# Performance work log

Measured on AMD Instinct MI355X. Metric: run time of the kernel, lower is better.

Reference implementation:

```python
import jax, jax.numpy as jnp
import numpy as np
from jax import lax


def setup_inputs() -> dict:
    key = jax.random.key(0)
    ks = jax.random.split(key, 6)
    B, S, V, E, H = 256, 512, 50000, 100, 512
    sentence = jax.random.randint(ks[0], (B, S), 0, V, dtype=jnp.int64)
    emb = jax.random.normal(ks[1], (V, E), dtype=jnp.float32)
    s = 1.0 / np.sqrt(H)
    W_ih = jax.random.normal(ks[2], (4 * H, E), dtype=jnp.float32) * s
    W_hh = jax.random.normal(ks[3], (4 * H, H), dtype=jnp.float32) * s
    b_ih = jax.random.normal(ks[4], (4 * H,), dtype=jnp.float32) * s
    b_hh = jax.random.normal(ks[5], (4 * H,), dtype=jnp.float32) * s
    return {"sentence": sentence, "emb": emb, "W_ih": W_ih, "W_hh": W_hh,
            "b_ih": b_ih, "b_hh": b_hh}


def reference(sentence, emb, W_ih, W_hh, b_ih, b_hh):
    # sentence: [B, S] int -> embed -> transpose to [S, B, E] (seq-major LSTM)
    x = jnp.take(emb, sentence, axis=0)            # [B, S, E]
    x = jnp.transpose(x, (1, 0, 2))                # [S, B, E]
    B = x.shape[1]
    H = W_hh.shape[1]
    # Precompute input contribution for all timesteps (big batched GEMM).
    # PyTorch gate layout along 4H axis: i, f, g, o.
    xg = jnp.einsum('sbe,ge->sbg', x, W_ih) + b_ih + b_hh  # [S, B, 4H]

    def step(carry, xt):
        h, c = carry
        gates = xt + h @ W_hh.T                    # [B, 4H]
        i, f, g, o = jnp.split(gates, 4, axis=-1)
        i = jax.nn.sigmoid(i)
        f = jax.nn.sigmoid(f)
        g = jnp.tanh(g)
        o = jax.nn.sigmoid(o)
        c = f * c + i * g
        h = o * jnp.tanh(c)
        return (h, c), None

    h0 = jnp.zeros((B, H), dtype=x.dtype)
    c0 = jnp.zeros((B, H), dtype=x.dtype)
    (hT, _), _ = lax.scan(step, (h0, c0), xg)
    # lstm_out[-1] is the hidden state at the final timestep.
    return hT
```

## Files before the change

### kernel.cpp

```cpp
#include <hip/hip_runtime.h>
#include <stdint.h>

#define B_  256
#define S_  512
#define E_  100
#define H_  512
#define G_  2048
#define KH_ 512

typedef _Float16 half8 __attribute__((ext_vector_type(8)));
typedef float    f32x4 __attribute__((ext_vector_type(4)));
union V16 { f32x4 f; half8 h; unsigned long long q[2]; };

#define OFF_WC   0u
#define OFF_HBT  2621440u
#define OFF_XB3  3670016u
#define OFF_XTL  28835840u
#define OFF_BIAS 29884416u
#define WS_NEED  29892608u

#define LDS_W   131072
#define LDS_A   16384
#define LDS_G   8448
#define LDS_TOT (LDS_W + LDS_A + LDS_G)

__global__ void prep_wc4(const float* __restrict__ Wih, const float* __restrict__ Whh,
                         const float* __restrict__ bih, const float* __restrict__ bhh,
                         _Float16* __restrict__ Wc, float* __restrict__ bias) {
    int idx = blockIdx.x * 256 + threadIdx.x;
    int e  = idx & 7;
    int L  = (idx >> 3) & 63;
    int q  = idx >> 9;
    int s  = q % 20;
    int qq = q / 20;
    int n  = qq & 1;
    int w  = (qq >> 1) & 3;
    int c  = qq >> 3;
    int g  = (w << 9) + (c << 5) + (n << 4) + (L & 15);
    int kl = ((L >> 4) << 3) + e;
    float v = 0.f;
    if (s < 16) {
        v = Whh[g * KH_ + (s << 5) + kl];
    } else {
        int xk = (s < 19) ? ((s - 16) << 5) + kl : 96 + kl;
        if (xk < E_) v = Wih[g * E_ + xk];
    }
    Wc[idx] = (_Float16)v;
    if (idx < G_) bias[idx] = bih[idx] + bhh[idx];
}

__global__ void prep_x3(const int* __restrict__ sent, const float* __restrict__ emb,
                        _Float16* __restrict__ xb3) {
    size_t idx = (size_t)blockIdx.x * 256 + threadIdx.x;
    int e  = (int)(idx & 7);
    int L  = (int)((idx >> 3) & 63);
    int q  = (int)(idx >> 9);
    int j  = q % 3;
    int qq = q / 3;
    int rg = qq & 15;
    int t  = qq >> 4;
    int b  = (rg << 4) + (L & 15);
    int k  = (j << 5) + ((L >> 4) << 3) + e;
    int tok = sent[b * S_ + t];
    xb3[idx] = (_Float16)emb[(size_t)tok * E_ + k];
}

__global__ void prep_xtail(const int* __restrict__ sent, const float* __restrict__ emb,
                           _Float16* __restrict__ xtl) {
    int idx = blockIdx.x * 256 + threadIdx.x;
    int e = idx & 3;
    int b = (idx >> 2) & 255;
    int t = idx >> 10;
    int tok = sent[b * S_ + t];
    xtl[idx] = (_Float16)emb[(size_t)tok * E_ + 96 + e];
}

__global__ __launch_bounds__(256, 1) void lstm_persist(
    const _Float16* __restrict__ Wc, unsigned long long* __restrict__ hbt,
    const _Float16* __restrict__ xb3, const _Float16* __restrict__ xtl,
    const float* __restrict__ bias, float* __restrict__ out)
{
    extern __shared__ __align__(16) char smem[];
    char* wl = smem;
    char* al = smem + LDS_W;
    float (*gbuf)[16][33] = reinterpret_cast<float(*)[16][33]>(smem + LDS_W + LDS_A);

    const int tid = threadIdx.x;
    const int L   = tid & 63;
    const int w   = tid >> 6;
    const int bx  = blockIdx.x;
    const int xcd = bx & 7;
    const int kk_ = bx >> 3;
    const int r   = (xcd << 1) | (kk_ >> 4);
    const int c   = kk_ & 15;
    const int brow0 = r << 4;
    const int hcol0 = c << 5;

    const _Float16* wp0 = Wc + (size_t)((((c << 2) + w) << 1)) * (20 * 512) + (L << 3);
    const _Float16* wp1 = wp0 + 20 * 512;
#pragma unroll
    for (int n = 0; n < 2; ++n)
#pragma unroll
        for (int kt = 0; kt < 16; ++kt) {
            f32x4 v = *reinterpret_cast<const f32x4*>((n ? wp1 : wp0) + (kt << 9));
            *reinterpret_cast<f32x4*>(wl + ((((w << 1) + n) * 16 + kt) << 10) + (L << 4)) = v;
        }
    V16 wx[2][4];
#pragma unroll
    for (int n = 0; n < 2; ++n)
#pragma unroll
        for (int j = 0; j < 4; ++j)
            wx[n][j].f = *reinterpret_cast<const f32x4*>((n ? wp1 : wp0) + ((16 + j) << 9));

    const int bl = tid >> 4;
    const int j0 = (tid << 1) & 31;
    const float bi0 = bias[hcol0 + j0],         bi1 = bias[hcol0 + j0 + 1];
    const float bf0 = bias[512  + hcol0 + j0],  bf1 = bias[512  + hcol0 + j0 + 1];
    const float bg0 = bias[1024 + hcol0 + j0],  bg1 = bias[1024 + hcol0 + j0 + 1];
    const float bo0 = bias[1536 + hcol0 + j0],  bo1 = bias[1536 + hcol0 + j0 + 1];
    float cc0 = 0.f, cc1 = 0.f;

    const int arow = L & 15;
    const int agrp = L >> 4;
    const int ard  = arow << 10;
    const int asw  = (arow & 7) << 4;

    V16 xf[3], xt;
    {
        const _Float16* xp = xb3 + ((size_t)r * 3) * 512 + (L << 3);
#pragma unroll
        for (int j = 0; j < 3; ++j) xf[j].f = *reinterpret_cast<const f32x4*>(xp + j * 512);
        unsigned long long tv = *reinterpret_cast<const unsigned long long*>(
            xtl + (size_t)(brow0 + arow) * 4);
        xt.q[0] = (agrp == 0) ? tv : 0ull;
        xt.q[1] = 0ull;
    }

    for (int t = 0; t < S_; ++t) {
        f32x4 a00 = {0,0,0,0}, a01 = {0,0,0,0}, a10 = {0,0,0,0}, a11 = {0,0,0,0};
#pragma unroll
        for (int j = 0; j < 4; ++j) {
            half8 a = (j < 3) ? xf[j].h : xt.h;
            if (j & 1) {
                a01 = __builtin_amdgcn_mfma_f32_16x16x32_f16(a, wx[0][j].h, a01, 0, 0, 0);
                a11 = __builtin_amdgcn_mfma_f32_16x16x32_f16(a, wx[1][j].h, a11, 0, 0, 0);
            } else {
                a00 = __builtin_amdgcn_mfma_f32_16x16x32_f16(a, wx[0][j].h, a00, 0, 0, 0);
                a10 = __builtin_amdgcn_mfma_f32_16x16x32_f16(a, wx[1][j].h, a10, 0, 0, 0);
            }
        }

        if (t > 0) {
            const unsigned long long* hq = hbt + ((size_t)(t & 1) << 16) + ((size_t)brow0 << 8);
            const unsigned tag = (unsigned)t;
            unsigned long long vv[16];
            int rounds = 0;
            bool again = true;
            while (again) {
#pragma unroll
                for (int j = 0; j < 16; ++j)
                    vv[j] = __hip_atomic_load(hq + (j << 8) + tid,
                                              __ATOMIC_RELAXED, __HIP_MEMORY_SCOPE_AGENT);
                again = false;
#pragma unroll
                for (int j = 0; j < 16; ++j) again |= ((unsigned)vv[j] != tag);
                if (++rounds > 4000000) break;
            }
            __builtin_amdgcn_sched_barrier(0);
#pragma unroll
            for (int j = 0; j < 16; ++j) {
                unsigned pack = (unsigned)(vv[j] >> 32);
                *reinterpret_cast<unsigned*>(
                    al + (j << 10) + ((((tid >> 2) ^ (j & 7))) << 4) + ((tid & 3) << 2)) = pack;
            }
        }
        __syncthreads();

        if (t > 0) {
#pragma unroll
            for (int kt = 0; kt < 16; ++kt) {
                V16 av, b0, b1;
                av.f = *reinterpret_cast<const f32x4*>(
                    al + ard + ((((kt << 2) + agrp) << 4) ^ asw));
                b0.f = *reinterpret_cast<const f32x4*>(wl + (((w << 5) + kt) << 10) + (L << 4));
                b1.f = *reinterpret_cast<const f32x4*>(wl + (((w << 5) + 16 + kt) << 10) + (L << 4));
                if (kt & 1) {
                    a01 = __builtin_amdgcn_mfma_f32_16x16x32_f16(av.h, b0.h, a01, 0, 0, 0);
                    a11 = __builtin_amdgcn_mfma_f32_16x16x32_f16(av.h, b1.h, a11, 0, 0, 0);
                } else {
                    a00 = __builtin_amdgcn_mfma_f32_16x16x32_f16(av.h, b0.h, a00, 0, 0, 0);
                    a10 = __builtin_amdgcn_mfma_f32_16x16x32_f16(av.h, b1.h, a10, 0, 0, 0);
                }
            }
        }
        f32x4 g0 = a00 + a01;
        f32x4 g1 = a10 + a11;
        {
            const int grb = agrp << 2;
            const int gc  = L & 15;
#pragma unroll
            for (int rr = 0; rr < 4; ++rr) {
                gbuf[w][grb + rr][gc]      = g0[rr];
                gbuf[w][grb + rr][16 + gc] = g1[rr];
            }
        }

        V16 xn[3], xnt;
        {
            const int tn = (t + 1) & (S_ - 1);
            const _Float16* xp = xb3 + (((size_t)tn * 16 + r) * 3) * 512 + (L << 3);
#pragma unroll
            for (int j = 0; j < 3; ++j) xn[j].f = *reinterpret_cast<const f32x4*>(xp + j * 512);
            unsigned long long tv = *reinterpret_cast<const unsigned long long*>(
                xtl + ((size_t)tn * 256 + brow0 + arow) * 4);
            xnt.q[0] = (agrp == 0) ? tv : 0ull;
            xnt.q[1] = 0ull;
        }
        __syncthreads();

        float i0 = gbuf[0][bl][j0]     + bi0, i1 = gbuf[0][bl][j0 + 1] + bi1;
        float f0 = gbuf[1][bl][j0]     + bf0, f1 = gbuf[1][bl][j0 + 1] + bf1;
        float gg0= gbuf[2][bl][j0]     + bg0, gg1= gbuf[2][bl][j0 + 1] + bg1;
        float o0 = gbuf[3][bl][j0]     + bo0, o1 = gbuf[3][bl][j0 + 1] + bo1;
        float si0 = 1.f / (1.f + __expf(-i0));
        float sf0 = 1.f / (1.f + __expf(-f0));
        float so0 = 1.f / (1.f + __expf(-o0));
        float tg0 = tanhf(gg0);
        float si1 = 1.f / (1.f + __expf(-i1));
        float sf1 = 1.f / (1.f + __expf(-f1));
        float so1 = 1.f / (1.f + __expf(-o1));
        float tg1 = tanhf(gg1);
        cc0 = sf0 * cc0 + si0 * tg0;
        cc1 = sf1 * cc1 + si1 * tg1;
        float h0 = so0 * tanhf(cc0);
        float h1 = so1 * tanhf(cc1);

        if (t == S_ - 1) {
            float* op = out + (size_t)(brow0 + bl) * H_ + hcol0 + j0;
            op[0] = h0; op[1] = h1;
        } else {
            _Float16 hh0 = (_Float16)h0, hh1 = (_Float16)h1;
            unsigned pack = ((unsigned)*(unsigned short*)&hh1 << 16)
                          |  (unsigned)*(unsigned short*)&hh0;
            unsigned long long word = ((unsigned long long)pack << 32)
                                    |  (unsigned long long)(unsigned)(t + 1);
            __hip_atomic_store(hbt + ((size_t)((t + 1) & 1) << 16)
                                   + ((size_t)(brow0 + bl) << 8) + (c << 4) + (tid & 15),
                               word, __ATOMIC_RELAXED, __HIP_MEMORY_SCOPE_AGENT);
        }

#pragma unroll
        for (int j = 0; j < 3; ++j) xf[j] = xn[j];
        xt = xnt;
    }
}

extern "C" void kernel_launch(void* const* d_in, const int* in_sizes, int n_in,
                              void* d_out, int out_size, void* d_ws, size_t ws_size,
                              hipStream_t stream) {
    (void)in_sizes; (void)n_in; (void)out_size;
    if (ws_size < WS_NEED) return;

    const int*   sent = (const int*)d_in[0];
    const float* emb  = (const float*)d_in[1];
    const float* Wih  = (const float*)d_in[2];
    const float* Whh  = (const float*)d_in[3];
    const float* bih  = (const float*)d_in[4];
    const float* bhh  = (const float*)d_in[5];

    char* ws = (char*)d_ws;
    _Float16*           Wc   = (_Float16*)(ws + OFF_WC);
    unsigned long long* hbt  = (unsigned long long*)(ws + OFF_HBT);
    _Float16*           xb3  = (_Float16*)(ws + OFF_XB3);
    _Float16*           xtl  = (_Float16*)(ws + OFF_XTL);
    float*              bias = (float*)(ws + OFF_BIAS);

    (void)hipFuncSetAttribute(reinterpret_cast<const void*>(lstm_persist),
                              hipFuncAttributeMaxDynamicSharedMemorySize, LDS_TOT);

    (void)hipMemsetAsync(hbt, 0, 2 * 256 * 256 * sizeof(unsigned long long), stream);

    prep_wc4<<<(16 * 4 * 2 * 20 * 64 * 8) / 256, 256, 0, stream>>>(Wih, Whh, bih, bhh, Wc, bias);
    prep_x3<<<(S_ * 16 * 3 * 512) / 256, 256, 0, stream>>>(sent, emb, xb3);
    prep_xtail<<<(S_ * B_ * 4) / 256, 256, 0, stream>>>(sent, emb, xtl);
    lstm_persist<<<256, 256, LDS_TOT, stream>>>(Wc, hbt, xb3, xtl, bias, (float*)d_out);
}
```

Baseline: 1.304 ms.

## Keep half of recurrent weights in registers and prefetch hidden-state polls early

Half of each wave's W_hh tiles (the first 8 k-steps) now stay in VGPRs and only the other half go to LDS, which halves LDS weight traffic per step and the LDS allocation. The hidden-state poll is restructured: the first load of the next step's h values is issued right after this step's store, a check runs before any reload, and s_sleep backs off between retries. The goal is to hide some of the cross-workgroup synchronisation latency and reduce polling pressure on memory, at the cost of higher register pressure and possible extra wake-up latency from the sleep.

```diff
diff --git a/kernel.cpp b/kernel.cpp
--- a/kernel.cpp
+++ b/kernel.cpp
@@ -19,7 +19,7 @@
 #define OFF_BIAS 29884416u
 #define WS_NEED  29892608u
 
-#define LDS_W   131072
+#define LDS_W   65536
 #define LDS_A   16384
 #define LDS_G   8448
 #define LDS_TOT (LDS_W + LDS_A + LDS_G)
@@ -75,7 +75,8 @@
     xtl[idx] = (_Float16)emb[(size_t)tok * E_ + 96 + e];
 }
 
-__global__ __launch_bounds__(256, 1) void lstm_persist(
+__global__ __launch_bounds__(256) __attribute__((amdgpu_waves_per_eu(1, 1)))
+void lstm_persist(
     const _Float16* __restrict__ Wc, unsigned long long* __restrict__ hbt,
     const _Float16* __restrict__ xb3, const _Float16* __restrict__ xtl,
     const float* __restrict__ bias, float* __restrict__ out)
@@ -98,13 +99,24 @@
 
     const _Float16* wp0 = Wc + (size_t)((((c << 2) + w) << 1)) * (20 * 512) + (L << 3);
     const _Float16* wp1 = wp0 + 20 * 512;
+    V16 wr[2][8];
 #pragma unroll
     for (int n = 0; n < 2; ++n)
 #pragma unroll
         for (int kt = 0; kt < 16; ++kt) {
             f32x4 v = *reinterpret_cast<const f32x4*>((n ? wp1 : wp0) + (kt << 9));
-            *reinterpret_cast<f32x4*>(wl + ((((w << 1) + n) * 16 + kt) << 10) + (L << 4)) = v;
-        }
+            if (kt < 8) {
+                wr[n][kt].f = v;
+            } else {
+                *reinterpret_cast<f32x4*>(
+                    wl + ((((w << 1) + n) << 3 | (kt - 8)) << 10) + (L << 4)) = v;
+            }
+        }
+#pragma unroll
+    for (int n = 0; n < 2; ++n)
+#pragma unroll
+        for (int kt = 0; kt < 8; ++kt)
+            asm volatile("" : "+v"(wr[n][kt].f));
     V16 wx[2][4];
 #pragma unroll
     for (int n = 0; n < 2; ++n)
@@ -135,6 +147,8 @@
         xt.q[0] = (agrp == 0) ? tv : 0ull;
         xt.q[1] = 0ull;
     }
+
+    unsigned long long vv[16];
 
     for (int t = 0; t < S_; ++t) {
         f32x4 a00 = {0,0,0,0}, a01 = {0,0,0,0}, a10 = {0,0,0,0}, a11 = {0,0,0,0};
@@ -153,18 +167,18 @@
         if (t > 0) {
             const unsigned long long* hq = hbt + ((size_t)(t & 1) << 16) + ((size_t)brow0 << 8);
             const unsigned tag = (unsigned)t;
-            unsigned long long vv[16];
             int rounds = 0;
-            bool again = true;
-            while (again) {
+            for (;;) {
+                bool again = false;
+#pragma unroll
+                for (int j = 0; j < 16; ++j) again |= ((unsigned)vv[j] != tag);
+                if (!again) break;
+                if (++rounds > 2000000) break;
+                __builtin_amdgcn_s_sleep(1);
 #pragma unroll
                 for (int j = 0; j < 16; ++j)
                     vv[j] = __hip_atomic_load(hq + (j << 8) + tid,
                                               __ATOMIC_RELAXED, __HIP_MEMORY_SCOPE_AGENT);
-                again = false;
-#pragma unroll
-                for (int j = 0; j < 16; ++j) again |= ((unsigned)vv[j] != tag);
-                if (++rounds > 4000000) break;
             }
             __builtin_amdgcn_sched_barrier(0);
 #pragma unroll
@@ -182,8 +196,15 @@
                 V16 av, b0, b1;
                 av.f = *reinterpret_cast<const f32x4*>(
                     al + ard + ((((kt << 2) + agrp) << 4) ^ asw));
-                b0.f = *reinterpret_cast<const f32x4*>(wl + (((w << 5) + kt) << 10) + (L << 4));
-                b1.f = *reinterpret_cast<const f32x4*>(wl + (((w << 5) + 16 + kt) << 10) + (L << 4));
+                if (kt < 8) {
+                    b0 = wr[0][kt];
+                    b1 = wr[1][kt];
+                } else {
+                    b0.f = *reinterpret_cast<const f32x4*>(
+                        wl + ((((w << 1) | 0) << 3 | (kt - 8)) << 10) + (L << 4));
+                    b1.f = *reinterpret_cast<const f32x4*>(
+                        wl + ((((w << 1) | 1) << 3 | (kt - 8)) << 10) + (L << 4));
+                }
                 if (kt & 1) {
                     a01 = __builtin_amdgcn_mfma_f32_16x16x32_f16(av.h, b0.h, a01, 0, 0, 0);
                     a11 = __builtin_amdgcn_mfma_f32_16x16x32_f16(av.h, b1.h, a11, 0, 0, 0);
@@ -247,6 +268,12 @@
             __hip_atomic_store(hbt + ((size_t)((t + 1) & 1) << 16)
                                    + ((size_t)(brow0 + bl) << 8) + (c << 4) + (tid & 15),
                                word, __ATOMIC_RELAXED, __HIP_MEMORY_SCOPE_AGENT);
+            const unsigned long long* hq2 = hbt + ((size_t)((t + 1) & 1) << 16)
+                                                + ((size_t)brow0 << 8);
+#pragma unroll
+            for (int j = 0; j < 16; ++j)
+                vv[j] = __hip_atomic_load(hq2 + (j << 8) + tid,
+                                          __ATOMIC_RELAXED, __HIP_MEMORY_SCOPE_AGENT);
         }
 
 #pragma unroll
```

Result: slower. 2.142 ms (+64.3%).

## Split each block over two row groups and overlap h exchange with compute

Applied to the files above, without the earlier changes.

Each persistent block now owns 16 hidden columns for two 16-row batch groups, where before it owned 32 columns for a single group. The two groups are processed in an interleaved pipeline: while one group's gate MFMAs and activations run, the other group's hidden state is prefetched with inline-asm cache-bypassing loads and checked against a tag, with a retry loop. The hidden-state exchange format shrinks to 32-bit words holding an fp16 value and a 16-bit tag, and the LDS weight footprint is halved. The intent is to hide cross-block synchronization latency behind compute, at the cost of more barriers per step and inline-asm memory-ordering risk.

```diff
diff --git a/kernel.cpp b/kernel.cpp
--- a/kernel.cpp
+++ b/kernel.cpp
@@ -10,7 +10,10 @@
 
 typedef _Float16 half8 __attribute__((ext_vector_type(8)));
 typedef float    f32x4 __attribute__((ext_vector_type(4)));
+typedef unsigned uint4v __attribute__((ext_vector_type(4)));
 union V16 { f32x4 f; half8 h; unsigned long long q[2]; };
+
+#define MFMA16 __builtin_amdgcn_mfma_f32_16x16x32_f16
 
 #define OFF_WC   0u
 #define OFF_HBT  2621440u
@@ -19,12 +22,72 @@
 #define OFF_BIAS 29884416u
 #define WS_NEED  29892608u
 
-#define LDS_W   131072
+#define LDS_W   65536
 #define LDS_A   16384
-#define LDS_G   8448
+#define LDS_G   4352
 #define LDS_TOT (LDS_W + LDS_A + LDS_G)
 
-__global__ void prep_wc4(const float* __restrict__ Wih, const float* __restrict__ Whh,
+#define GL8(v, b)                                                       \
+  asm volatile(                                                         \
+    "global_load_dwordx4 %0, %8, off sc0 sc1\n\t"                       \
+    "global_load_dwordx4 %1, %9, off sc0 sc1\n\t"                       \
+    "global_load_dwordx4 %2, %10, off sc0 sc1\n\t"                      \
+    "global_load_dwordx4 %3, %11, off sc0 sc1\n\t"                      \
+    "global_load_dwordx4 %4, %12, off sc0 sc1\n\t"                      \
+    "global_load_dwordx4 %5, %13, off sc0 sc1\n\t"                      \
+    "global_load_dwordx4 %6, %14, off sc0 sc1\n\t"                      \
+    "global_load_dwordx4 %7, %15, off sc0 sc1"                          \
+    : "=&v"(v[0]), "=&v"(v[1]), "=&v"(v[2]), "=&v"(v[3]),               \
+      "=&v"(v[4]), "=&v"(v[5]), "=&v"(v[6]), "=&v"(v[7])                \
+    : "v"(b), "v"(b + 4096), "v"(b + 8192), "v"(b + 12288),             \
+      "v"(b + 16384), "v"(b + 20480), "v"(b + 24576), "v"(b + 28672)    \
+    : "memory")
+
+#define GL8W(v, b)                                                      \
+  asm volatile(                                                         \
+    "global_load_dwordx4 %0, %8, off sc0 sc1\n\t"                       \
+    "global_load_dwordx4 %1, %9, off sc0 sc1\n\t"                       \
+    "global_load_dwordx4 %2, %10, off sc0 sc1\n\t"                      \
+    "global_load_dwordx4 %3, %11, off sc0 sc1\n\t"                      \
+    "global_load_dwordx4 %4, %12, off sc0 sc1\n\t"                      \
+    "global_load_dwordx4 %5, %13, off sc0 sc1\n\t"                      \
+    "global_load_dwordx4 %6, %14, off sc0 sc1\n\t"                      \
+    "global_load_dwordx4 %7, %15, off sc0 sc1\n\t"                      \
+    "s_waitcnt vmcnt(0)"                                                \
+    : "=&v"(v[0]), "=&v"(v[1]), "=&v"(v[2]), "=&v"(v[3]),               \
+      "=&v"(v[4]), "=&v"(v[5]), "=&v"(v[6]), "=&v"(v[7])                \
+    : "v"(b), "v"(b + 4096), "v"(b + 8192), "v"(b + 12288),             \
+      "v"(b + 16384), "v"(b + 20480), "v"(b + 24576), "v"(b + 28672)    \
+    : "memory")
+
+#define VWAIT8(v)                                                       \
+  asm volatile("s_waitcnt vmcnt(0)"                                     \
+    : "+v"(v[0]), "+v"(v[1]), "+v"(v[2]), "+v"(v[3]),                   \
+      "+v"(v[4]), "+v"(v[5]), "+v"(v[6]), "+v"(v[7]) :: "memory")
+
+static __device__ __forceinline__ void validate_retry(uint4v* v, const char* base,
+                                                      unsigned tag) {
+    VWAIT8(v);
+    __builtin_amdgcn_sched_barrier(0);
+    unsigned bad = 0;
+#pragma unroll
+    for (int i = 0; i < 8; ++i)
+#pragma unroll
+        for (int k = 0; k < 4; ++k) bad |= (v[i][k] ^ tag) & 0xFFFFu;
+    int r = 0;
+    while (__any(bad != 0)) {
+        if (++r > 2000000) break;
+        GL8W(v, base);
+        bad = 0;
+#pragma unroll
+        for (int i = 0; i < 8; ++i)
+#pragma unroll
+            for (int k = 0; k < 4; ++k) bad |= (v[i][k] ^ tag) & 0xFFFFu;
+    }
+    __builtin_amdgcn_sched_barrier(0);
+}
+
+__global__ void prep_wc5(const float* __restrict__ Wih, const float* __restrict__ Whh,
                          const float* __restrict__ bih, const float* __restrict__ bhh,
                          _Float16* __restrict__ Wc, float* __restrict__ bias) {
     int idx = blockIdx.x * 256 + threadIdx.x;
@@ -32,11 +95,10 @@
     int L  = (idx >> 3) & 63;
     int q  = idx >> 9;
     int s  = q % 20;
-    int qq = q / 20;
-    int n  = qq & 1;
-    int w  = (qq >> 1) & 3;
-    int c  = qq >> 3;
-    int g  = (w << 9) + (c << 5) + (n << 4) + (L & 15);
+    int r1 = q / 20;
+    int w  = r1 & 3;
+    int c  = r1 >> 2;
+    int g  = (w << 9) + (c << 4) + (L & 15);
     int kl = ((L >> 4) << 3) + e;
     float v = 0.f;
     if (s < 16) {
@@ -76,183 +138,217 @@
 }
 
 __global__ __launch_bounds__(256, 1) void lstm_persist(
-    const _Float16* __restrict__ Wc, unsigned long long* __restrict__ hbt,
+    const _Float16* __restrict__ Wc, unsigned* __restrict__ hbt,
     const _Float16* __restrict__ xb3, const _Float16* __restrict__ xtl,
     const float* __restrict__ bias, float* __restrict__ out)
 {
     extern __shared__ __align__(16) char smem[];
     char* wl = smem;
     char* al = smem + LDS_W;
-    float (*gbuf)[16][33] = reinterpret_cast<float(*)[16][33]>(smem + LDS_W + LDS_A);
+    float (*gbuf)[16][17] = reinterpret_cast<float(*)[16][17]>(smem + LDS_W + LDS_A);
 
     const int tid = threadIdx.x;
     const int L   = tid & 63;
     const int w   = tid >> 6;
     const int bx  = blockIdx.x;
-    const int xcd = bx & 7;
-    const int kk_ = bx >> 3;
-    const int r   = (xcd << 1) | (kk_ >> 4);
-    const int c   = kk_ & 15;
-    const int brow0 = r << 4;
-    const int hcol0 = c << 5;
-
-    const _Float16* wp0 = Wc + (size_t)((((c << 2) + w) << 1)) * (20 * 512) + (L << 3);
-    const _Float16* wp1 = wp0 + 20 * 512;
-#pragma unroll
-    for (int n = 0; n < 2; ++n)
-#pragma unroll
-        for (int kt = 0; kt < 16; ++kt) {
-            f32x4 v = *reinterpret_cast<const f32x4*>((n ? wp1 : wp0) + (kt << 9));
-            *reinterpret_cast<f32x4*>(wl + ((((w << 1) + n) * 16 + kt) << 10) + (L << 4)) = v;
-        }
-    V16 wx[2][4];
-#pragma unroll
-    for (int n = 0; n < 2; ++n)
-#pragma unroll
-        for (int j = 0; j < 4; ++j)
-            wx[n][j].f = *reinterpret_cast<const f32x4*>((n ? wp1 : wp0) + ((16 + j) << 9));
-
-    const int bl = tid >> 4;
-    const int j0 = (tid << 1) & 31;
-    const float bi0 = bias[hcol0 + j0],         bi1 = bias[hcol0 + j0 + 1];
-    const float bf0 = bias[512  + hcol0 + j0],  bf1 = bias[512  + hcol0 + j0 + 1];
-    const float bg0 = bias[1024 + hcol0 + j0],  bg1 = bias[1024 + hcol0 + j0 + 1];
-    const float bo0 = bias[1536 + hcol0 + j0],  bo1 = bias[1536 + hcol0 + j0 + 1];
-    float cc0 = 0.f, cc1 = 0.f;
+    const int rp  = bx & 7;
+    const int c16 = bx >> 3;
+    const int rA  = rp, rB = rp + 8;
+    const int hcol0 = c16 << 4;
+
+    const _Float16* wp = Wc + (size_t)((c16 << 2) + w) * (20 * 512) + (L << 3);
+#pragma unroll
+    for (int s = 0; s < 16; ++s)
+        *reinterpret_cast<f32x4*>(wl + (((w << 4) + s) << 10) + (L << 4)) =
+            *reinterpret_cast<const f32x4*>(wp + (s << 9));
+    V16 wx[4];
+#pragma unroll
+    for (int j = 0; j < 4; ++j)
+        wx[j].f = *reinterpret_cast<const f32x4*>(wp + ((16 + j) << 9));
+
+    const int eb = tid >> 4;
+    const int ej = tid & 15;
+    const int hcol = hcol0 + ej;
+    const float bi = bias[hcol], bf = bias[512 + hcol];
+    const float bg = bias[1024 + hcol], bo = bias[1536 + hcol];
+    float csA = 0.f, csB = 0.f;
 
     const int arow = L & 15;
     const int agrp = L >> 4;
     const int ard  = arow << 10;
     const int asw  = (arow & 7) << 4;
 
-    V16 xf[3], xt;
+    V16 xfA[3], xtA, xfB[3], xtB, xnA[3], xntA, xnB[3], xntB;
     {
-        const _Float16* xp = xb3 + ((size_t)r * 3) * 512 + (L << 3);
-#pragma unroll
-        for (int j = 0; j < 3; ++j) xf[j].f = *reinterpret_cast<const f32x4*>(xp + j * 512);
-        unsigned long long tv = *reinterpret_cast<const unsigned long long*>(
-            xtl + (size_t)(brow0 + arow) * 4);
-        xt.q[0] = (agrp == 0) ? tv : 0ull;
-        xt.q[1] = 0ull;
+        const _Float16* xpA = xb3 + ((size_t)rA * 3) * 512 + (L << 3);
+        const _Float16* xpB = xb3 + ((size_t)rB * 3) * 512 + (L << 3);
+#pragma unroll
+        for (int j = 0; j < 3; ++j) {
+            xfA[j].f = *reinterpret_cast<const f32x4*>(xpA + j * 512);
+            xfB[j].f = *reinterpret_cast<const f32x4*>(xpB + j * 512);
+        }
+        unsigned long long tvA = *reinterpret_cast<const unsigned long long*>(
+            xtl + (size_t)(rA * 16 + arow) * 4);
+        unsigned long long tvB = *reinterpret_cast<const unsigned long long*>(
+            xtl + (size_t)(rB * 16 + arow) * 4);
+        xtA.q[0] = (agrp == 0) ? tvA : 0ull;  xtA.q[1] = 0ull;
+        xtB.q[0] = (agrp == 0) ? tvB : 0ull;  xtB.q[1] = 0ull;
     }
 
+    uint4v vA[8] = {}, vB[8] = {};
+
+#define STAGE8(v)                                                            \
+    do {                                                                     \
+        _Pragma("unroll")                                                    \
+        for (int i = 0; i < 8; ++i) {                                        \
+            int b_ = (i << 1) + (tid >> 7);                                  \
+            unsigned lo = (v[i][0] >> 16) | (v[i][1] & 0xFFFF0000u);         \
+            unsigned hi = (v[i][2] >> 16) | (v[i][3] & 0xFFFF0000u);         \
+            unsigned long long val = ((unsigned long long)hi << 32) | lo;    \
+            *reinterpret_cast<unsigned long long*>(                          \
+                al + (b_ << 10) +                                            \
+                (((((tid & 127) >> 1) << 4) ^ ((b_ & 7) << 4))) +            \
+                ((tid & 1) << 3)) = val;                                     \
+        }                                                                    \
+    } while (0)
+
     for (int t = 0; t < S_; ++t) {
-        f32x4 a00 = {0,0,0,0}, a01 = {0,0,0,0}, a10 = {0,0,0,0}, a11 = {0,0,0,0};
-#pragma unroll
-        for (int j = 0; j < 4; ++j) {
-            half8 a = (j < 3) ? xf[j].h : xt.h;
-            if (j & 1) {
-                a01 = __builtin_amdgcn_mfma_f32_16x16x32_f16(a, wx[0][j].h, a01, 0, 0, 0);
-                a11 = __builtin_amdgcn_mfma_f32_16x16x32_f16(a, wx[1][j].h, a11, 0, 0, 0);
+        const char* baseA_t  = (const char*)hbt + ((size_t)(t & 1) << 19)
+                             + ((size_t)rA << 15) + (tid << 4);
+        const char* baseB_t  = (const char*)hbt + ((size_t)(t & 1) << 19)
+                             + ((size_t)rB << 15) + (tid << 4);
+        const unsigned tag = (unsigned)t;
+
+        if (t > 0) { validate_retry(vA, baseA_t, tag); STAGE8(vA); }
+        __syncthreads();
+        if (t > 0) { GL8(vB, baseB_t); __builtin_amdgcn_sched_barrier(0); }
+
+        {
+            f32x4 a0 = {0,0,0,0}, a1 = {0,0,0,0};
+#pragma unroll
+            for (int j = 0; j < 4; ++j) {
+                half8 a = (j < 3) ? xfA[j].h : xtA.h;
+                if (j & 1) a1 = MFMA16(a, wx[j].h, a1, 0, 0, 0);
+                else       a0 = MFMA16(a, wx[j].h, a0, 0, 0, 0);
+            }
+            if (t > 0) {
+#pragma unroll
+                for (int kt = 0; kt < 16; ++kt) {
+                    V16 av, bv;
+                    av.f = *reinterpret_cast<const f32x4*>(
+                        al + ard + ((((kt << 2) + agrp) << 4) ^ asw));
+                    bv.f = *reinterpret_cast<const f32x4*>(
+                        wl + (((w << 4) + kt) << 10) + (L << 4));
+                    if (kt & 1) a1 = MFMA16(av.h, bv.h, a1, 0, 0, 0);
+                    else        a0 = MFMA16(av.h, bv.h, a0, 0, 0, 0);
+                }
+            }
+            f32x4 g = a0 + a1;
+            const int grb = agrp << 2, gc = L & 15;
+#pragma unroll
+            for (int rr = 0; rr < 4; ++rr) gbuf[w][grb + rr][gc] = g[rr];
+        }
+        __syncthreads();
+
+        {
+            float iv = gbuf[0][eb][ej] + bi, fv = gbuf[1][eb][ej] + bf;
+            float gv = gbuf[2][eb][ej] + bg, ov = gbuf[3][eb][ej] + bo;
+            float si = 1.f / (1.f + __expf(-iv));
+            float sf = 1.f / (1.f + __expf(-fv));
+            float so = 1.f / (1.f + __expf(-ov));
+            float tg = tanhf(gv);
+            csA = sf * csA + si * tg;
+            float hv = so * tanhf(csA);
+            if (t == S_ - 1) {
+                out[(size_t)(rA * 16 + eb) * H_ + hcol] = hv;
             } else {
-                a00 = __builtin_amdgcn_mfma_f32_16x16x32_f16(a, wx[0][j].h, a00, 0, 0, 0);
-                a10 = __builtin_amdgcn_mfma_f32_16x16x32_f16(a, wx[1][j].h, a10, 0, 0, 0);
-            }
-        }
-
-        if (t > 0) {
-            const unsigned long long* hq = hbt + ((size_t)(t & 1) << 16) + ((size_t)brow0 << 8);
-            const unsigned tag = (unsigned)t;
-            unsigned long long vv[16];
-            int rounds = 0;
-            bool again = true;
-            while (again) {
-#pragma unroll
-                for (int j = 0; j < 16; ++j)
-                    vv[j] = __hip_atomic_load(hq + (j << 8) + tid,
-                                              __ATOMIC_RELAXED, __HIP_MEMORY_SCOPE_AGENT);
-                again = false;
-#pragma unroll
-                for (int j = 0; j < 16; ++j) again |= ((unsigned)vv[j] != tag);
-                if (++rounds > 4000000) break;
-            }
+                _Float16 hh = (_Float16)hv;
+                unsigned word = ((unsigned)*(unsigned short*)&hh << 16)
+                              | (unsigned)(t + 1);
+                __hip_atomic_store(hbt + ((size_t)((t + 1) & 1) << 17)
+                                       + ((size_t)rA << 13) + (eb << 9) + hcol,
+                                   word, __ATOMIC_RELAXED, __HIP_MEMORY_SCOPE_AGENT);
+            }
+        }
+
+        if (t > 0) { validate_retry(vB, baseB_t, tag); STAGE8(vB); }
+        __syncthreads();
+        if (t < S_ - 1) {
+            const char* baseA_n = (const char*)hbt + ((size_t)((t + 1) & 1) << 19)
+                                + ((size_t)rA << 15) + (tid << 4);
+            GL8(vA, baseA_n);
             __builtin_amdgcn_sched_barrier(0);
-#pragma unroll
-            for (int j = 0; j < 16; ++j) {
-                unsigned pack = (unsigned)(vv[j] >> 32);
-                *reinterpret_cast<unsigned*>(
-                    al + (j << 10) + ((((tid >> 2) ^ (j & 7))) << 4) + ((tid & 3) << 2)) = pack;
-            }
+        }
+        {
+            const int tn = (t + 1) & (S_ - 1);
+            const _Float16* xpA = xb3 + (((size_t)tn * 16 + rA) * 3) * 512 + (L << 3);
+            const _Float16* xpB = xb3 + (((size_t)tn * 16 + rB) * 3) * 512 + (L << 3);
+#pragma unroll
+            for (int j = 0; j < 3; ++j) {
+                xnA[j].f = *reinterpret_cast<const f32x4*>(xpA + j * 512);
+                xnB[j].f = *reinterpret_cast<const f32x4*>(xpB + j * 512);
+            }
+            unsigned long long tvA = *reinterpret_cast<const unsigned long long*>(
+                xtl + ((size_t)tn * 256 + rA * 16 + arow) * 4);
+            unsigned long long tvB = *reinterpret_cast<const unsigned long long*>(
+                xtl + ((size_t)tn * 256 + rB * 16 + arow) * 4);
+            xntA.q[0] = (agrp == 0) ? tvA : 0ull;  xntA.q[1] = 0ull;
+            xntB.q[0] = (agrp == 0) ? tvB : 0ull;  xntB.q[1] = 0ull;
+        }
+
+        {
+            f32x4 a0 = {0,0,0,0}, a1 = {0,0,0,0};
+#pragma unroll
+            for (int j = 0; j < 4; ++j) {
+                half8 a = (j < 3) ? xfB[j].h : xtB.h;
+                if (j & 1) a1 = MFMA16(a, wx[j].h, a1, 0, 0, 0);
+                else       a0 = MFMA16(a, wx[j].h, a0, 0, 0, 0);
+            }
+            if (t > 0) {
+#pragma unroll
+                for (int kt = 0; kt < 16; ++kt) {
+                    V16 av, bv;
+                    av.f = *reinterpret_cast<const f32x4*>(
+                        al + ard + ((((kt << 2) + agrp) << 4) ^ asw));
+                    bv.f = *reinterpret_cast<const f32x4*>(
+                        wl + (((w << 4) + kt) << 10) + (L << 4));
+                    if (kt & 1) a1 = MFMA16(av.h, bv.h, a1, 0, 0, 0);
+                    else        a0 = MFMA16(av.h, bv.h, a0, 0, 0, 0);
+                }
+            }
+            f32x4 g = a0 + a1;
+            const int grb = agrp << 2, gc = L & 15;
+#pragma unroll
+            for (int rr = 0; rr < 4; ++rr) gbuf[w][grb + rr][gc] = g[rr];
         }
         __syncthreads();
 
-        if (t > 0) {
-#pragma unroll
-            for (int kt = 0; kt < 16; ++kt) {
-                V16 av, b0, b1;
-                av.f = *reinterpret_cast<const f32x4*>(
-                    al + ard + ((((kt << 2) + agrp) << 4) ^ asw));
-                b0.f = *reinterpret_cast<const f32x4*>(wl + (((w << 5) + kt) << 10) + (L << 4));
-                b1.f = *reinterpret_cast<const f32x4*>(wl + (((w << 5) + 16 + kt) << 10) + (L << 4));
-                if (kt & 1) {
-                    a01 = __builtin_amdgcn_mfma_f32_16x16x32_f16(av.h, b0.h, a01, 0, 0, 0);
-                    a11 = __builtin_amdgcn_mfma_f32_16x16x32_f16(av.h, b1.h, a11, 0, 0, 0);
-                } else {
-                    a00 = __builtin_amdgcn_mfma_f32_16x16x32_f16(av.h, b0.h, a00, 0, 0, 0);
-                    a10 = __builtin_amdgcn_mfma_f32_16x16x32_f16(av.h, b1.h, a10, 0, 0, 0);
-                }
-            }
-        }
-        f32x4 g0 = a00 + a01;
-        f32x4 g1 = a10 + a11;
-        {
-            const int grb = agrp << 2;
-            const int gc  = L & 15;
-#pragma unroll
-            for (int rr = 0; rr < 4; ++rr) {
-                gbuf[w][grb + rr][gc]      = g0[rr];
-                gbuf[w][grb + rr][16 + gc] = g1[rr];
-            }
-        }
-
-        V16 xn[3], xnt;
-        {
-            const int tn = (t + 1) & (S_ - 1);
-            const _Float16* xp = xb3 + (((size_t)tn * 16 + r) * 3) * 512 + (L << 3);
-#pragma unroll
-            for (int j = 0; j < 3; ++j) xn[j].f = *reinterpret_cast<const f32x4*>(xp + j * 512);
-            unsigned long long tv = *reinterpret_cast<const unsigned long long*>(
-                xtl + ((size_t)tn * 256 + brow0 + arow) * 4);
-            xnt.q[0] = (agrp == 0) ? tv : 0ull;
-            xnt.q[1] = 0ull;
-        }
-        __syncthreads();
-
-        float i0 = gbuf[0][bl][j0]     + bi0, i1 = gbuf[0][bl][j0 + 1] + bi1;
-        float f0 = gbuf[1][bl][j0]     + bf0, f1 = gbuf[1][bl][j0 + 1] + bf1;
-        float gg0= gbuf[2][bl][j0]     + bg0, gg1= gbuf[2][bl][j0 + 1] + bg1;
-        float o0 = gbuf[3][bl][j0]     + bo0, o1 = gbuf[3][bl][j0 + 1] + bo1;
-        float si0 = 1.f / (1.f + __expf(-i0));
-        float sf0 = 1.f / (1.f + __expf(-f0));
-        float so0 = 1.f / (1.f + __expf(-o0));
-        float tg0 = tanhf(gg0);
-        float si1 = 1.f / (1.f + __expf(-i1));
-        float sf1 = 1.f / (1.f + __expf(-f1));
-        float so1 = 1.f / (1.f + __expf(-o1));
-        float tg1 = tanhf(gg1);
-        cc0 = sf0 * cc0 + si0 * tg0;
-        cc1 = sf1 * cc1 + si1 * tg1;
-        float h0 = so0 * tanhf(cc0);
-        float h1 = so1 * tanhf(cc1);
-
-        if (t == S_ - 1) {
-            float* op = out + (size_t)(brow0 + bl) * H_ + hcol0 + j0;
-            op[0] = h0; op[1] = h1;
-        } else {
-            _Float16 hh0 = (_Float16)h0, hh1 = (_Float16)h1;
-            unsigned pack = ((unsigned)*(unsigned short*)&hh1 << 16)
-                          |  (unsigned)*(unsigned short*)&hh0;
-            unsigned long long word = ((unsigned long long)pack << 32)
-                                    |  (unsigned long long)(unsigned)(t + 1);
-            __hip_atomic_store(hbt + ((size_t)((t + 1) & 1) << 16)
-                                   + ((size_t)(brow0 + bl) << 8) + (c << 4) + (tid & 15),
-                               word, __ATOMIC_RELAXED, __HIP_MEMORY_SCOPE_AGENT);
-        }
-
-#pragma unroll
-        for (int j = 0; j < 3; ++j) xf[j] = xn[j];
-        xt = xnt;
+        {
+            float iv = gbuf[0][eb][ej] + bi, fv = gbuf[1][eb][ej] + bf;
+            float gv = gbuf[2][eb][ej] + bg, ov = gbuf[3][eb][ej] + bo;
+            float si = 1.f / (1.f + __expf(-iv));
+            float sf = 1.f / (1.f + __expf(-fv));
+            float so = 1.f / (1.f + __expf(-ov));
+            float tg = tanhf(gv);
+            csB = sf * csB + si * tg;
+            float hv = so * tanhf(csB);
+            if (t == S_ - 1) {
+                out[(size_t)(rB * 16 + eb) * H_ + hcol] = hv;
+            } else {
+                _Float16 hh = (_Float16)hv;
+                unsigned word = ((unsigned)*(unsigned short*)&hh << 16)
+                              | (unsigned)(t + 1);
+                __hip_atomic_store(hbt + ((size_t)((t + 1) & 1) << 17)
+                                       + ((size_t)rB << 13) + (eb << 9) + hcol,
+                                   word, __ATOMIC_RELAXED, __HIP_MEMORY_SCOPE_AGENT);
+            }
+        }
+
+#pragma unroll
+        for (int j = 0; j < 3; ++j) { xfA[j] = xnA[j]; xfB[j] = xnB[j]; }
+        xtA = xntA;  xtB = xntB;
     }
+#undef STAGE8
 }
 
 extern "C" void kernel_launch(void* const* d_in, const int* in_sizes, int n_in,
@@ -269,19 +365,19 @@
     const float* bhh  = (const float*)d_in[5];
 
     char* ws = (char*)d_ws;
-    _Float16*           Wc   = (_Float16*)(ws + OFF_WC);
-    unsigned long long* hbt  = (unsigned long long*)(ws + OFF_HBT);
-    _Float16*           xb3  = (_Float16*)(ws + OFF_XB3);
-    _Float16*           xtl  = (_Float16*)(ws + OFF_XTL);
-    float*              bias = (float*)(ws + OFF_BIAS);
+    _Float16* Wc   = (_Float16*)(ws + OFF_WC);
+    unsigned* hbt  = (unsigned*)(ws + OFF_HBT);
+    _Float16* xb3  = (_Float16*)(ws + OFF_XB3);
+    _Float16* xtl  = (_Float16*)(ws + OFF_XTL);
+    float*    bias = (float*)(ws + OFF_BIAS);
 
     (void)hipFuncSetAttribute(reinterpret_cast<const void*>(lstm_persist),
                               hipFuncAttributeMaxDynamicSharedMemorySize, LDS_TOT);
 
-    (void)hipMemsetAsync(hbt, 0, 2 * 256 * 256 * sizeof(unsigned long long), stream);
-
-    prep_wc4<<<(16 * 4 * 2 * 20 * 64 * 8) / 256, 256, 0, stream>>>(Wih, Whh, bih, bhh, Wc, bias);
-    prep_x3<<<(S_ * 16 * 3 * 512) / 256, 256, 0, stream>>>(sent, emb, xb3);
-    prep_xtail<<<(S_ * B_ * 4) / 256, 256, 0, stream>>>(sent, emb, xtl);
+    (void)hipMemsetAsync(hbt, 0, 1048576, stream);
+
+    prep_wc5<<<5120, 256, 0, stream>>>(Wih, Whh, bih, bhh, Wc, bias);
+    prep_x3<<<49152, 256, 0, stream>>>(sent, emb, xb3);
+    prep_xtail<<<2048, 256, 0, stream>>>(sent, emb, xtl);
     lstm_persist<<<256, 256, LDS_TOT, stream>>>(Wc, hbt, xb3, xtl, bias, (float*)d_out);
 }
```

After: 2.123 ms. +62.8%, slower.
